# Performance work log

Measured on AMD Instinct MI355X. Metric: run time of the kernel, lower is better.

The kernel has to match this reference:

```python
import jax, jax.numpy as jnp
import numpy as np

N_NODES = 50000
N_EDGES = 200000
H = 128
L = 6
NODE_IN = 9
EDGE_IN = 10
OUT = 3


def _glorot(key, shape):
    fan_in = shape[0]
    return jax.random.normal(key, shape, dtype=jnp.float32) * (1.0 / np.sqrt(fan_in))


def setup_inputs() -> dict:
    key = jax.random.key(0)
    ks = jax.random.split(key, 32)
    x = jax.random.normal(ks[0], (N_NODES, NODE_IN), dtype=jnp.float32)
    edge_attr = jax.random.normal(ks[1], (N_EDGES, EDGE_IN), dtype=jnp.float32)
    edge_index = jax.random.randint(ks[2], (2, N_EDGES), 0, N_NODES, dtype=jnp.int32)
    bc_disp = (jax.random.uniform(ks[3], (N_NODES, 2)) < 0.05).astype(jnp.float32)
    bc_rot = (jax.random.uniform(ks[4], (N_NODES, 1)) < 0.05).astype(jnp.float32)
    inp = {
        'x': x, 'edge_attr': edge_attr, 'edge_index': edge_index,
        'bc_disp': bc_disp, 'bc_rot': bc_rot,
        # node encoder MLP(NODE_IN,[H],H)
        'enc_n_W1': _glorot(ks[5], (NODE_IN, H)), 'enc_n_b1': jnp.zeros((H,), jnp.float32),
        'enc_n_W2': _glorot(ks[6], (H, H)), 'enc_n_b2': jnp.zeros((H,), jnp.float32),
        # edge encoder MLP(EDGE_IN,[H],H)
        'enc_e_W1': _glorot(ks[7], (EDGE_IN, H)), 'enc_e_b1': jnp.zeros((H,), jnp.float32),
        'enc_e_W2': _glorot(ks[8], (H, H)), 'enc_e_b2': jnp.zeros((H,), jnp.float32),
        # L message-passing layers: msg MLP(3H->H->H), update MLP(2H->H->H), stacked on dim 0
        'mp_msg_W1': jnp.stack([_glorot(jax.random.fold_in(ks[9], i), (3 * H, H)) for i in range(L)]),
        'mp_msg_b1': jnp.zeros((L, H), jnp.float32),
        'mp_msg_W2': jnp.stack([_glorot(jax.random.fold_in(ks[10], i), (H, H)) for i in range(L)]),
        'mp_msg_b2': jnp.zeros((L, H), jnp.float32),
        'mp_upd_W1': jnp.stack([_glorot(jax.random.fold_in(ks[11], i), (2 * H, H)) for i in range(L)]),
        'mp_upd_b1': jnp.zeros((L, H), jnp.float32),
        'mp_upd_W2': jnp.stack([_glorot(jax.random.fold_in(ks[12], i), (H, H)) for i in range(L)]),
        'mp_upd_b2': jnp.zeros((L, H), jnp.float32),
        # decoder MLP(H,[H,64],OUT)
        'dec_W1': _glorot(ks[13], (H, H)), 'dec_b1': jnp.zeros((H,), jnp.float32),
        'dec_W2': _glorot(ks[14], (H, 64)), 'dec_b2': jnp.zeros((64,), jnp.float32),
        'dec_W3': _glorot(ks[15], (64, OUT)), 'dec_b3': jnp.zeros((OUT,), jnp.float32),
    }
    return inp


def _pignn_forward(x, edge_attr, edge_index, bc_disp, bc_rot,
                   enc_n_W1, enc_n_b1, enc_n_W2, enc_n_b2,
                   enc_e_W1, enc_e_b1, enc_e_W2, enc_e_b2,
                   mp_msg_W1, mp_msg_b1, mp_msg_W2, mp_msg_b2,
                   mp_upd_W1, mp_upd_b1, mp_upd_W2, mp_upd_b2,
                   dec_W1, dec_b1, dec_W2, dec_b2, dec_W3, dec_b3):
    relu = jax.nn.relu
    n = x.shape[0]
    src, dst = edge_index[0], edge_index[1]

    # encoders: Linear -> ReLU -> Linear
    h = relu(x @ enc_n_W1 + enc_n_b1) @ enc_n_W2 + enc_n_b2            # [N, H]
    e = relu(edge_attr @ enc_e_W1 + enc_e_b1) @ enc_e_W2 + enc_e_b2    # [E, H]

    def mp_step(h, params):
        mW1, mb1, mW2, mb2, uW1, ub1, uW2, ub2 = params
        m_in = jnp.concatenate([h[src], h[dst], e], axis=-1)           # [E, 3H]
        m = relu(m_in @ mW1 + mb1) @ mW2 + mb2                         # [E, H]
        agg = jax.ops.segment_sum(m, dst, num_segments=n)              # [N, H]
        u_in = jnp.concatenate([h, agg], axis=-1)                      # [N, 2H]
        upd = relu(u_in @ uW1 + ub1) @ uW2 + ub2                       # [N, H]
        return h + upd, None                                           # residual

    h, _ = jax.lax.scan(mp_step, h,
                        (mp_msg_W1, mp_msg_b1, mp_msg_W2, mp_msg_b2,
                         mp_upd_W1, mp_upd_b1, mp_upd_W2, mp_upd_b2))

    # decoder: H -> H -> 64 -> OUT with ReLU between layers
    d = relu(h @ dec_W1 + dec_b1)
    d = relu(d @ dec_W2 + dec_b2)
    pred = d @ dec_W3 + dec_b3                                         # [N, 3]

    # hard boundary conditions
    disp_mask = 1.0 - bc_disp
    rot_mask = 1.0 - bc_rot
    return jnp.concatenate([pred[:, 0:2] * disp_mask, pred[:, 2:3] * rot_mask], axis=1)


def reference(x, edge_attr, edge_index, bc_disp, bc_rot,
              enc_n_W1, enc_n_b1, enc_n_W2, enc_n_b2,
              enc_e_W1, enc_e_b1, enc_e_W2, enc_e_b2,
              mp_msg_W1, mp_msg_b1, mp_msg_W2, mp_msg_b2,
              mp_upd_W1, mp_upd_b1, mp_upd_W2, mp_upd_b2,
              dec_W1, dec_b1, dec_W2, dec_b2, dec_W3, dec_b3):
    return _pignn_forward(x, edge_attr, edge_index, bc_disp, bc_rot,
                          enc_n_W1, enc_n_b1, enc_n_W2, enc_n_b2,
                          enc_e_W1, enc_e_b1, enc_e_W2, enc_e_b2,
                          mp_msg_W1, mp_msg_b1, mp_msg_W2, mp_msg_b2,
                          mp_upd_W1, mp_upd_b1, mp_upd_W2, mp_upd_b2,
                          dec_W1, dec_b1, dec_W2, dec_b2, dec_W3, dec_b3)
```

## Files before the change

kernel.cpp:

```cpp
#include <hip/hip_runtime.h>

#define NN 50000
#define NE 200000
#define HD 128

typedef unsigned short us4 __attribute__((ext_vector_type(4)));
typedef unsigned short us8 __attribute__((ext_vector_type(8)));
typedef short s8 __attribute__((ext_vector_type(8)));
typedef float f4 __attribute__((ext_vector_type(4)));

#define SA 136
#define SA32 40
#define SC2 68

__device__ __forceinline__ float b2f(unsigned short u) {
    union { unsigned i; float f; } v; v.i = ((unsigned)u) << 16; return v.f;
}
__device__ __forceinline__ unsigned short f2b(float x) {
    union { float f; unsigned i; } v; v.f = x;
    unsigned r = v.i + 0x7fffu + ((v.i >> 16) & 1u);
    return (unsigned short)(r >> 16);
}
struct hl2 { short hi, lo; };
__device__ __forceinline__ hl2 split2(float x) {
    unsigned short h = f2b(x);
    hl2 r;
    r.hi = (short)h;
    r.lo = (short)f2b(x - b2f(h));
    return r;
}

__global__ __launch_bounds__(256) void zeroi_k(int* __restrict__ p, int n) {
    int i = blockIdx.x * 256 + threadIdx.x;
    if (i < n) p[i] = 0;
}
__global__ __launch_bounds__(256) void zerof_k(float* __restrict__ p, long n) {
    long i = (long)blockIdx.x * 256 + threadIdx.x;
    if (i < n) p[i] = 0.f;
}

__global__ __launch_bounds__(256) void hist_k(const int* __restrict__ dst, int* __restrict__ cnt) {
    int i = blockIdx.x * 256 + threadIdx.x;
    if (i < NE) atomicAdd(&cnt[dst[i]], 1);
}
__global__ __launch_bounds__(256) void scan1_k(const int* __restrict__ cnt, int* __restrict__ bsum) {
    __shared__ int sc[256];
    int i = blockIdx.x * 256 + threadIdx.x;
    sc[threadIdx.x] = (i < NN) ? cnt[i] : 0;
    __syncthreads();
    for (int off = 128; off > 0; off >>= 1) {
        if (threadIdx.x < off) sc[threadIdx.x] += sc[threadIdx.x + off];
        __syncthreads();
    }
    if (threadIdx.x == 0) bsum[blockIdx.x] = sc[0];
}
__global__ __launch_bounds__(256) void scan2_k(int* __restrict__ bsum, int nb) {
    __shared__ int sc[256];
    int t = threadIdx.x;
    int v = (t < nb) ? bsum[t] : 0;
    sc[t] = v;
    __syncthreads();
    for (int off = 1; off < 256; off <<= 1) {
        int a = (t >= off) ? sc[t - off] : 0;
        __syncthreads();
        sc[t] += a;
        __syncthreads();
    }
    if (t < nb) bsum[t] = sc[t] - v;
}
__global__ __launch_bounds__(256) void scan3_k(const int* __restrict__ cnt, const int* __restrict__ bsum,
                                               int* __restrict__ rp, float* __restrict__ deg) {
    __shared__ int sc[256];
    int t = threadIdx.x;
    int i = blockIdx.x * 256 + t;
    int v = (i < NN) ? cnt[i] : 0;
    sc[t] = v;
    __syncthreads();
    for (int off = 1; off < 256; off <<= 1) {
        int a = (t >= off) ? sc[t - off] : 0;
        __syncthreads();
        sc[t] += a;
        __syncthreads();
    }
    int incl = sc[t];
    if (i < NN) {
        rp[i] = bsum[blockIdx.x] + incl - v;
        deg[i] = (float)v;
        if (i == NN - 1) rp[NN] = bsum[blockIdx.x] + incl;
    }
}
__global__ __launch_bounds__(256) void posbuild_k(const int* __restrict__ src, const int* __restrict__ dst,
                                                  const int* __restrict__ rp, int* __restrict__ cur,
                                                  int* __restrict__ pos, int* __restrict__ srcS,
                                                  int* __restrict__ dstS) {
    int i = blockIdx.x * 256 + threadIdx.x;
    if (i >= NE) return;
    int d = dst[i];
    int p = rp[d] + atomicAdd(&cur[d], 1);
    pos[i] = p;
    srcS[p] = src[i];
    dstS[p] = d;
}

__global__ __launch_bounds__(256) void mini_k(const float* __restrict__ W2m, const float* __restrict__ uW1b,
                                              const float* __restrict__ b2m,
                                              float* __restrict__ W2u, float* __restrict__ b2u) {
    int r = blockIdx.x * 16 + (threadIdx.x >> 4);
    int c0 = (threadIdx.x & 15) * 8;
    float a[8] = {};
    for (int k = 0; k < HD; ++k) {
        float w = W2m[r * HD + k];
        const float* u = uW1b + k * HD + c0;
        float4 u0 = *(const float4*)u, u1 = *(const float4*)(u + 4);
        a[0] = fmaf(w, u0.x, a[0]); a[1] = fmaf(w, u0.y, a[1]);
        a[2] = fmaf(w, u0.z, a[2]); a[3] = fmaf(w, u0.w, a[3]);
        a[4] = fmaf(w, u1.x, a[4]); a[5] = fmaf(w, u1.y, a[5]);
        a[6] = fmaf(w, u1.z, a[6]); a[7] = fmaf(w, u1.w, a[7]);
    }
    *(float4*)(W2u + r * HD + c0)     = float4{a[0], a[1], a[2], a[3]};
    *(float4*)(W2u + r * HD + c0 + 4) = float4{a[4], a[5], a[6], a[7]};
    if (blockIdx.x == 0 && threadIdx.x < 16) {
        int cc = threadIdx.x * 8;
        float b[8] = {};
        for (int k = 0; k < HD; ++k) {
            float w = b2m[k];
            const float* u = uW1b + k * HD + cc;
            float4 u0 = *(const float4*)u, u1 = *(const float4*)(u + 4);
            b[0] = fmaf(w, u0.x, b[0]); b[1] = fmaf(w, u0.y, b[1]);
            b[2] = fmaf(w, u0.z, b[2]); b[3] = fmaf(w, u0.w, b[3]);
            b[4] = fmaf(w, u1.x, b[4]); b[5] = fmaf(w, u1.y, b[5]);
            b[6] = fmaf(w, u1.z, b[6]); b[7] = fmaf(w, u1.w, b[7]);
        }
        *(float4*)(b2u + cc)     = float4{b[0], b[1], b[2], b[3]};
        *(float4*)(b2u + cc + 4) = float4{b[4], b[5], b[6], b[7]};
    }
}
__global__ __launch_bounds__(256) void wtL_k(const float* __restrict__ msgW1, const float* __restrict__ updW1,
                                             const float* __restrict__ updW2, const float* __restrict__ W2uF,
                                             unsigned short* __restrict__ dst) {
    int idx = blockIdx.x * 256 + threadIdx.x;
    int m = idx >> 14;
    int r = idx & 16383;
    int n = r >> 7, k = r & 127;
    float v;
    switch (m) {
        case 0: v = msgW1[(long)k * HD + n]; break;
        case 1: v = msgW1[(long)(128 + k) * HD + n]; break;
        case 2: v = msgW1[(long)(256 + k) * HD + n]; break;
        case 3: v = updW1[(long)k * HD + n]; break;
        case 4: v = updW2[(long)k * HD + n]; break;
        default: v = W2uF[(long)k * HD + n]; break;
    }
    hl2 p = split2(v);
    dst[(long)m * 32768 + n * HD + k] = (unsigned short)p.hi;
    dst[(long)m * 32768 + 16384 + n * HD + k] = (unsigned short)p.lo;
}
__global__ __launch_bounds__(256) void wtE_k(const float* __restrict__ nW1, const float* __restrict__ nW2,
                                             const float* __restrict__ eW1, const float* __restrict__ eW2,
                                             unsigned short* __restrict__ dst) {
    int idx = blockIdx.x * 256 + threadIdx.x;
    float v; long off; int pos, sz;
    if (idx < 4096) {
        int n = idx >> 5, k = idx & 31;
        v = (k < 9) ? nW1[k * HD + n] : 0.f; off = 0; pos = idx; sz = 4096;
    } else if (idx < 20480) {
        int r = idx - 4096; int n = r >> 7, k = r & 127;
        v = nW2[k * HD + n]; off = 8192; pos = r; sz = 16384;
    } else if (idx < 24576) {
        int r = idx - 20480; int n = r >> 5, k = r & 31;
        v = (k < 10) ? eW1[k * HD + n] : 0.f; off = 40960; pos = r; sz = 4096;
    } else {
        int r = idx - 24576; int n = r >> 7, k = r & 127;
        v = eW2[k * HD + n]; off = 49152; pos = r; sz = 16384;
    }
    hl2 p = split2(v);
    dst[off + pos] = (unsigned short)p.hi;
    dst[off + sz + pos] = (unsigned short)p.lo;
}
__global__ __launch_bounds__(256) void wtD_k(const float* __restrict__ dW1, const float* __restrict__ dW2,
                                             unsigned short* __restrict__ dst) {
    int idx = blockIdx.x * 256 + threadIdx.x;
    if (idx < 16384) {
        int n = idx >> 7, k = idx & 127;
        hl2 p = split2(dW1[k * HD + n]);
        dst[idx] = (unsigned short)p.hi;
        dst[16384 + idx] = (unsigned short)p.lo;
    } else {
        int r = idx - 16384;
        int n = r >> 7, k = r & 127;
        hl2 p = split2(dW2[k * 64 + n]);
        dst[32768 + r] = (unsigned short)p.hi;
        dst[40960 + r] = (unsigned short)p.lo;
    }
}

__device__ __forceinline__ void stageA_f32_split(short* __restrict__ At, short* __restrict__ Al,
                                                 const float* __restrict__ A, int bm, int M, int tid) {
#pragma unroll
    for (int t = 0; t < 4; ++t) {
        int c = tid + t * 256;
        int row = c >> 4, k8 = (c & 15) * 8;
        int gr = bm + row;
        s8 vh = (s8)0, vl = (s8)0;
        if (gr < M) {
            const float* p = A + (long)gr * HD + k8;
            f4 a = *(const f4*)p, b = *(const f4*)(p + 4);
#pragma unroll
            for (int i = 0; i < 4; ++i) {
                hl2 pa = split2(a[i]);
                hl2 pb = split2(b[i]);
                vh[i] = pa.hi; vl[i] = pa.lo;
                vh[4 + i] = pb.hi; vl[4 + i] = pb.lo;
            }
        }
        *(s8*)(At + row * SA + k8) = vh;
        *(s8*)(Al + row * SA + k8) = vl;
    }
}
__device__ __forceinline__ void stageA_b16(short* __restrict__ At, const unsigned short* __restrict__ A,
                                           int bm, int M, int tid) {
#pragma unroll
    for (int t = 0; t < 4; ++t) {
        int c = tid + t * 256;
        int row = c >> 4, k8 = (c & 15) * 8;
        int gr = bm + row;
        s8 v = (s8)0;
        if (gr < M) v = *(const s8*)(A + (long)gr * HD + k8);
        *(s8*)(At + row * SA + k8) = v;
    }
}
__device__ __forceinline__ void loadB2(s8 b[2][4], const unsigned short* __restrict__ W,
                                       int sw, int nk, int w, int lane) {
    const int r16 = lane & 15, q8 = (lane >> 4) * 8;
#pragma unroll
    for (int ct = 0; ct < 2; ++ct)
#pragma unroll 4
        for (int ks = 0; ks < nk; ++ks)
            b[ct][ks] = *(const s8*)((const short*)W + (long)((2 * w + ct) * 16 + r16) * sw + ks * 32 + q8);
}
__device__ __forceinline__ void mfma3_reg(f4 acc[4][2], const short* __restrict__ At,
                                          const short* __restrict__ Al, int sa,
                                          const s8 bh[2][4], const s8 bl[2][4], int nk, int lane) {
    const int r16 = lane & 15, q8 = (lane >> 4) * 8;
#pragma unroll 4
    for (int ks = 0; ks < nk; ++ks)
#pragma unroll
        for (int rt = 0; rt < 4; ++rt) {
            s8 ah = *(const s8*)(At + (rt * 16 + r16) * sa + ks * 32 + q8);
            s8 al = *(const s8*)(Al + (rt * 16 + r16) * sa + ks * 32 + q8);
#pragma unroll
            for (int ct = 0; ct < 2; ++ct) {
                acc[rt][ct] = __builtin_amdgcn_mfma_f32_16x16x32_bf16(ah, bh[ct][ks], acc[rt][ct], 0, 0, 0);
                acc[rt][ct] = __builtin_amdgcn_mfma_f32_16x16x32_bf16(al, bh[ct][ks], acc[rt][ct], 0, 0, 0);
                acc[rt][ct] = __builtin_amdgcn_mfma_f32_16x16x32_bf16(ah, bl[ct][ks], acc[rt][ct], 0, 0, 0);
            }
        }
}
__device__ __forceinline__ void mfmaE_reg(f4 acc[4][2], const short* __restrict__ At, int sa,
                                          const s8 bh[2][4], const s8 bl[2][4], int nk, int lane) {
    const int r16 = lane & 15, q8 = (lane >> 4) * 8;
#pragma unroll 4
    for (int ks = 0; ks < nk; ++ks)
#pragma unroll
        for (int rt = 0; rt < 4; ++rt) {
            s8 a = *(const s8*)(At + (rt * 16 + r16) * sa + ks * 32 + q8);
#pragma unroll
            for (int ct = 0; ct < 2; ++ct) {
                acc[rt][ct] = __builtin_amdgcn_mfma_f32_16x16x32_bf16(a, bh[ct][ks], acc[rt][ct], 0, 0, 0);
                acc[rt][ct] = __builtin_amdgcn_mfma_f32_16x16x32_bf16(a, bl[ct][ks], acc[rt][ct], 0, 0, 0);
            }
        }
}
__device__ __forceinline__ void dumpC_half2(float* __restrict__ Cd, const f4 acc[4][2],
                                            int half, int w, int lane) {
    if ((w >> 1) != half) return;
    const int col0 = lane & 15, rq = (lane >> 4) * 4;
    const int bc = (w & 1) * 2;
#pragma unroll
    for (int rt = 0; rt < 4; ++rt)
#pragma unroll
        for (int ct = 0; ct < 2; ++ct)
#pragma unroll
            for (int r = 0; r < 4; ++r)
                Cd[(rt * 16 + rq + r) * SC2 + (bc + ct) * 16 + col0] = acc[rt][ct][r];
}
#define ACC_ZERO2(acc) { f4 z_ = {0.f, 0.f, 0.f, 0.f}; \
    for (int r_ = 0; r_ < 4; ++r_) for (int c_ = 0; c_ < 2; ++c_) acc[r_][c_] = z_; }

__device__ __forceinline__ void stageA32_f32(short* __restrict__ At, short* __restrict__ Al,
                                             const float* __restrict__ A, int bm, int M, int tid) {
#pragma unroll
    for (int t = 0; t < 2; ++t) {
        int c = tid + t * 256;
        int row = c >> 4, k8 = (c & 15) * 8;
        int gr = bm + row;
        s8 vh = (s8)0, vl = (s8)0;
        if (gr < M) {
            const float* p = A + (long)gr * HD + k8;
            f4 a = *(const f4*)p, b = *(const f4*)(p + 4);
#pragma unroll
            for (int i = 0; i < 4; ++i) {
                hl2 pa = split2(a[i]);
                hl2 pb = split2(b[i]);
                vh[i] = pa.hi; vl[i] = pa.lo;
                vh[4 + i] = pb.hi; vl[4 + i] = pb.lo;
            }
        }
        *(s8*)(At + row * SA + k8) = vh;
        *(s8*)(Al + row * SA + k8) = vl;
    }
}
__device__ __forceinline__ void stage_segsum32(short* __restrict__ At, short* __restrict__ Al,
                                               const unsigned short* __restrict__ Pe,
                                               const int* __restrict__ rowp,
                                               int bm, int M, int tid) {
#pragma unroll
    for (int t = 0; t < 2; ++t) {
        int c = tid + t * 256;
        int row = c >> 4, k8 = (c & 15) * 8;
        int gr = bm + row;
        float sum[8] = {};
        if (gr < M) {
            int e0 = rowp[gr], e1 = rowp[gr + 1];
            int e = e0;
            for (; e + 2 <= e1; e += 2) {
                us8 v0 = *(const us8*)(Pe + (long)e * HD + k8);
                us8 v1 = *(const us8*)(Pe + (long)(e + 1) * HD + k8);
#pragma unroll
                for (int i = 0; i < 8; ++i) sum[i] += b2f(v0[i]) + b2f(v1[i]);
            }
            if (e < e1) {
                us8 v = *(const us8*)(Pe + (long)e * HD + k8);
#pragma unroll
                for (int i = 0; i < 8; ++i) sum[i] += b2f(v[i]);
            }
        }
        s8 vh, vl;
#pragma unroll
        for (int i = 0; i < 8; ++i) {
            hl2 p = split2(sum[i]);
            vh[i] = p.hi; vl[i] = p.lo;
        }
        *(s8*)(At + row * SA + k8) = vh;
        *(s8*)(Al + row * SA + k8) = vl;
    }
}
__device__ __forceinline__ void mfma3_reg32(f4 acc[2][2], const short* __restrict__ At,
                                            const short* __restrict__ Al,
                                            const s8 bh[2][4], const s8 bl[2][4], int lane) {
    const int r16 = lane & 15, q8 = (lane >> 4) * 8;
#pragma unroll
    for (int ks = 0; ks < 4; ++ks)
#pragma unroll
        for (int rt = 0; rt < 2; ++rt) {
            s8 ah = *(const s8*)(At + (rt * 16 + r16) * SA + ks * 32 + q8);
            s8 al = *(const s8*)(Al + (rt * 16 + r16) * SA + ks * 32 + q8);
#pragma unroll
            for (int ct = 0; ct < 2; ++ct) {
                acc[rt][ct] = __builtin_amdgcn_mfma_f32_16x16x32_bf16(ah, bh[ct][ks], acc[rt][ct], 0, 0, 0);
                acc[rt][ct] = __builtin_amdgcn_mfma_f32_16x16x32_bf16(al, bh[ct][ks], acc[rt][ct], 0, 0, 0);
                acc[rt][ct] = __builtin_amdgcn_mfma_f32_16x16x32_bf16(ah, bl[ct][ks], acc[rt][ct], 0, 0, 0);
            }
        }
}
__device__ __forceinline__ void dumpC32(float* __restrict__ Cd, const f4 acc[2][2],
                                        int half, int w, int lane) {
    if ((w >> 1) != half) return;
    const int col0 = lane & 15, rq = (lane >> 4) * 4;
    const int bc = (w & 1) * 2;
#pragma unroll
    for (int rt = 0; rt < 2; ++rt)
#pragma unroll
        for (int ct = 0; ct < 2; ++ct)
#pragma unroll
            for (int r = 0; r < 4; ++r)
                Cd[(rt * 16 + rq + r) * SC2 + (bc + ct) * 16 + col0] = acc[rt][ct][r];
}
#define ACC_ZERO22(acc) { f4 z_ = {0.f, 0.f, 0.f, 0.f}; \
    for (int r_ = 0; r_ < 2; ++r_) for (int c_ = 0; c_ < 2; ++c_) acc[r_][c_] = z_; }

__global__ __launch_bounds__(256) void dual_k(const float* __restrict__ h,
                                              const unsigned short* __restrict__ W1aT,
                                              const unsigned short* __restrict__ W1bT,
                                              unsigned short* __restrict__ Hs, unsigned short* __restrict__ Hd,
                                              int M) {
    __shared__ __align__(16) short At[64 * SA];
    __shared__ __align__(16) short Al[64 * SA];
    __shared__ __align__(16) float Cd[64 * SC2];
    const int tid = threadIdx.x, lane = tid & 63, w = tid >> 6, tx = tid & 15, ty = tid >> 4;
    const int bm = blockIdx.x * 64;
    s8 bh[2][4], bl[2][4];
    loadB2(bh, W1aT, HD, 4, w, lane);
    loadB2(bl, W1aT + 16384, HD, 4, w, lane);
    stageA_f32_split(At, Al, h, bm, M, tid);
    __syncthreads();
    f4 acc[4][2]; ACC_ZERO2(acc);
    mfma3_reg(acc, At, Al, SA, bh, bl, 4, lane);
    loadB2(bh, W1bT, HD, 4, w, lane);
    loadB2(bl, W1bT + 16384, HD, 4, w, lane);
#pragma unroll
    for (int half = 0; half < 2; ++half) {
        __syncthreads();
        dumpC_half2(Cd, acc, half, w, lane);
        __syncthreads();
        int c4 = half * 64 + tx * 4;
#pragma unroll
        for (int i = 0; i < 4; ++i) {
            int row = ty * 4 + i, gr = bm + row;
            if (gr >= M) continue;
            f4 v = *(const f4*)(Cd + row * SC2 + tx * 4);
            us4 o;
#pragma unroll
            for (int j = 0; j < 4; ++j) o[j] = f2b(v[j]);
            *(us4*)(Hs + (long)gr * HD + c4) = o;
        }
    }
    ACC_ZERO2(acc);
    mfma3_reg(acc, At, Al, SA, bh, bl, 4, lane);
#pragma unroll
    for (int half = 0; half < 2; ++half) {
        __syncthreads();
        dumpC_half2(Cd, acc, half, w, lane);
        __syncthreads();
        int c4 = half * 64 + tx * 4;
#pragma unroll
        for (int i = 0; i < 4; ++i) {
            int row = ty * 4 + i, gr = bm + row;
            if (gr >= M) continue;
            f4 v = *(const f4*)(Cd + row * SC2 + tx * 4);
            us4 o;
#pragma unroll
            for (int j = 0; j < 4; ++j) o[j] = f2b(v[j]);
            *(us4*)(Hd + (long)gr * HD + c4) = o;
        }
    }
}

__global__ __launch_bounds__(256) void edge_k(const unsigned short* __restrict__ eS,
                                              const unsigned short* __restrict__ Hs,
                                              const unsigned short* __restrict__ Hd,
                                              const int* __restrict__ srcS, const int* __restrict__ dstS,
                                              const unsigned short* __restrict__ W1cT,
                                              const float* __restrict__ b1,
                                              unsigned short* __restrict__ Pe) {
    __shared__ __align__(16) short At[64 * SA];
    __shared__ __align__(16) float Cd[64 * SC2];
    const int tid = threadIdx.x, lane = tid & 63, w = tid >> 6, tx = tid & 15, ty = tid >> 4;
    const int bm = blockIdx.x * 64;
    s8 bh[2][4], bl[2][4];
    loadB2(bh, W1cT, HD, 4, w, lane);
    loadB2(bl, W1cT + 16384, HD, 4, w, lane);
    stageA_b16(At, eS, bm, NE, tid);
    __syncthreads();
    f4 acc[4][2]; ACC_ZERO2(acc);
    mfmaE_reg(acc, At, SA, bh, bl, 4, lane);
#pragma unroll
    for (int half = 0; half < 2; ++half) {
        __syncthreads();
        dumpC_half2(Cd, acc, half, w, lane);
        __syncthreads();
        int c4 = half * 64 + tx * 4;
        f4 bv = *(const f4*)(b1 + c4);
#pragma unroll
        for (int i = 0; i < 4; ++i) {
            int row = ty * 4 + i, edge = bm + row;
            int s = srcS[edge], d = dstS[edge];
            us4 hs = *(const us4*)(Hs + (long)s * HD + c4);
            us4 hd = *(const us4*)(Hd + (long)d * HD + c4);
            f4 cv = *(const f4*)(Cd + row * SC2 + tx * 4);
            us4 o;
#pragma unroll
            for (int j = 0; j < 4; ++j)
                o[j] = f2b(fmaxf(cv[j] + bv[j] + b2f(hs[j]) + b2f(hd[j]), 0.f));
            *(us4*)(Pe + (long)edge * HD + c4) = o;
        }
    }
}

__global__ __launch_bounds__(256) void upd_k(float* __restrict__ h,
                                             const unsigned short* __restrict__ Pe,
                                             const int* __restrict__ rowp,
                                             const unsigned short* __restrict__ uW1aT,
                                             const unsigned short* __restrict__ W2uT,
                                             const float* __restrict__ ub1, const float* __restrict__ b2u,
                                             const float* __restrict__ deg,
                                             const unsigned short* __restrict__ uW2T,
                                             const float* __restrict__ ub2,
                                             const unsigned short* __restrict__ W1aTn,
                                             const unsigned short* __restrict__ W1bTn,
                                             unsigned short* __restrict__ Hs,
                                             unsigned short* __restrict__ Hd, int M) {
    __shared__ __align__(16) short At[32 * SA];
    __shared__ __align__(16) short Al[32 * SA];
    __shared__ __align__(16) float Cd[32 * SC2];
    const int tid = threadIdx.x, lane = tid & 63, w = tid >> 6, tx = tid & 15, ty = tid >> 4;
    const int bm = blockIdx.x * 32;
    const int col0 = lane & 15, rq = (lane >> 4) * 4;
    s8 bh[2][4], bl[2][4];
    f4 acc[2][2]; ACC_ZERO22(acc);
    loadB2(bh, uW1aT, HD, 4, w, lane);
    loadB2(bl, uW1aT + 16384, HD, 4, w, lane);
    stageA32_f32(At, Al, h, bm, M, tid);
    __syncthreads();
    mfma3_reg32(acc, At, Al, bh, bl, lane);
    loadB2(bh, W2uT, HD, 4, w, lane);
    loadB2(bl, W2uT + 16384, HD, 4, w, lane);
    __syncthreads();
    stage_segsum32(At, Al, Pe, rowp, bm, M, tid);
    __syncthreads();
    mfma3_reg32(acc, At, Al, bh, bl, lane);
    loadB2(bh, uW2T, HD, 4, w, lane);
    loadB2(bl, uW2T + 16384, HD, 4, w, lane);
    __syncthreads();
    {
        float u1[2], u2[2];
#pragma unroll
        for (int ct = 0; ct < 2; ++ct) {
            int col = (2 * w + ct) * 16 + col0;
            u1[ct] = ub1[col]; u2[ct] = b2u[col];
        }
        float dgv[8];
#pragma unroll
        for (int rt = 0; rt < 2; ++rt)
#pragma unroll
            for (int r = 0; r < 4; ++r) {
                int gr = bm + rt * 16 + rq + r;
                dgv[rt * 4 + r] = (gr < M) ? deg[gr] : 0.f;
            }
#pragma unroll
        for (int rt = 0; rt < 2; ++rt)
#pragma unroll
            for (int ct = 0; ct < 2; ++ct)
#pragma unroll
                for (int r = 0; r < 4; ++r) {
                    float p = fmaxf(acc[rt][ct][r] + u1[ct] + dgv[rt * 4 + r] * u2[ct], 0.f);
                    hl2 pp = split2(p);
                    int off = (rt * 16 + rq + r) * SA + (2 * w + ct) * 16 + col0;
                    At[off] = pp.hi;
                    Al[off] = pp.lo;
                }
    }
    __syncthreads();
    ACC_ZERO22(acc);
    mfma3_reg32(acc, At, Al, bh, bl, lane);
    if (W1aTn) {
        loadB2(bh, W1aTn, HD, 4, w, lane);
        loadB2(bl, W1aTn + 16384, HD, 4, w, lane);
    }
    __syncthreads();
#pragma unroll
    for (int half = 0; half < 2; ++half) {
        __syncthreads();
        dumpC32(Cd, acc, half, w, lane);
        __syncthreads();
        int c4 = half * 64 + tx * 4;
        f4 u0 = *(const f4*)(ub2 + c4);
#pragma unroll
        for (int i = 0; i < 2; ++i) {
            int row = ty * 2 + i, gr = bm + row;
            if (gr >= M) continue;
            float* hp = h + (long)gr * HD + c4;
            f4 a = *(f4*)hp;
            f4 cv = *(const f4*)(Cd + row * SC2 + tx * 4);
#pragma unroll
            for (int j = 0; j < 4; ++j) a[j] += cv[j] + u0[j];
            *(f4*)hp = a;
#pragma unroll
            for (int j = 0; j < 4; ++j) {
                hl2 pp = split2(a[j]);
                At[row * SA + c4 + j] = pp.hi;
                Al[row * SA + c4 + j] = pp.lo;
            }
        }
    }
    if (!W1aTn) return;
    __syncthreads();
    ACC_ZERO22(acc);
    mfma3_reg32(acc, At, Al, bh, bl, lane);
    loadB2(bh, W1bTn, HD, 4, w, lane);
    loadB2(bl, W1bTn + 16384, HD, 4, w, lane);
#pragma unroll
    for (int half = 0; half < 2; ++half) {
        __syncthreads();
        dumpC32(Cd, acc, half, w, lane);
        __syncthreads();
        int c4 = half * 64 + tx * 4;
#pragma unroll
        for (int i = 0; i < 2; ++i) {
            int row = ty * 2 + i, gr = bm + row;
            if (gr >= M) continue;
            f4 v = *(const f4*)(Cd + row * SC2 + tx * 4);
            us4 o;
#pragma unroll
            for (int j = 0; j < 4; ++j) o[j] = f2b(v[j]);
            *(us4*)(Hs + (long)gr * HD + c4) = o;
        }
    }
    ACC_ZERO22(acc);
    mfma3_reg32(acc, At, Al, bh, bl, lane);
#pragma unroll
    for (int half = 0; half < 2; ++half) {
        __syncthreads();
        dumpC32(Cd, acc, half, w, lane);
        __syncthreads();
        int c4 = half * 64 + tx * 4;
#pragma unroll
        for (int i = 0; i < 2; ++i) {
            int row = ty * 2 + i, gr = bm + row;
            if (gr >= M) continue;
            f4 v = *(const f4*)(Cd + row * SC2 + tx * 4);
            us4 o;
#pragma unroll
            for (int j = 0; j < 4; ++j) o[j] = f2b(v[j]);
            *(us4*)(Hd + (long)gr * HD + c4) = o;
        }
    }
}

template<bool SCAT>
__global__ __launch_bounds__(256) void enc_k(const float* __restrict__ A, int KIN,
                                             const unsigned short* __restrict__ W1T, const float* __restrict__ b1,
                                             const unsigned short* __restrict__ W2T, const float* __restrict__ b2,
                                             float* __restrict__ outF, unsigned short* __restrict__ outB,
                                             const int* __restrict__ pos, int M) {
    __shared__ __align__(16) short At[64 * SA];
    __shared__ __align__(16) short Al[64 * SA];
    float* Cd = (float*)At;
    const int tid = threadIdx.x, lane = tid & 63, w = tid >> 6, tx = tid & 15, ty = tid >> 4;
    const int bm = blockIdx.x * 64;
    s8 bh[2][4], bl[2][4];
    loadB2(bh, W1T, 32, 1, w, lane);
    loadB2(bl, W1T + 4096, 32, 1, w, lane);
    {
        int row = tid >> 2, k8 = (tid & 3) * 8;
        int gr = bm + row;
        s8 vh = (s8)0, vl = (s8)0;
        if (gr < M) {
#pragma unroll
            for (int i = 0; i < 8; ++i) {
                int k = k8 + i;
                if (k < KIN) {
                    hl2 p = split2(A[(long)gr * KIN + k]);
                    vh[i] = p.hi; vl[i] = p.lo;
                }
            }
        }
        *(s8*)(At + row * SA32 + k8) = vh;
        *(s8*)(Al + row * SA32 + k8) = vl;
    }
    __syncthreads();
    f4 acc[4][2]; ACC_ZERO2(acc);
    mfma3_reg(acc, At, Al, SA32, bh, bl, 1, lane);
    loadB2(bh, W2T, HD, 4, w, lane);
    loadB2(bl, W2T + 16384, HD, 4, w, lane);
    __syncthreads();
    {
        const int col0 = lane & 15, rq = (lane >> 4) * 4;
        float bb[2];
#pragma unroll
        for (int ct = 0; ct < 2; ++ct) bb[ct] = b1[(2 * w + ct) * 16 + col0];
#pragma unroll
        for (int rt = 0; rt < 4; ++rt)
#pragma unroll
            for (int ct = 0; ct < 2; ++ct)
#pragma unroll
                for (int r = 0; r < 4; ++r) {
                    float p = fmaxf(acc[rt][ct][r] + bb[ct], 0.f);
                    hl2 pp = split2(p);
                    int off = (rt * 16 + rq + r) * SA + (2 * w + ct) * 16 + col0;
                    At[off] = pp.hi;
                    Al[off] = pp.lo;
                }
    }
    __syncthreads();
    ACC_ZERO2(acc);
    mfma3_reg(acc, At, Al, SA, bh, bl, 4, lane);
#pragma unroll
    for (int half = 0; half < 2; ++half) {
        __syncthreads();
        dumpC_half2(Cd, acc, half, w, lane);
        __syncthreads();
        int c4 = half * 64 + tx * 4;
        f4 bv = *(const f4*)(b2 + c4);
#pragma unroll
        for (int i = 0; i < 4; ++i) {
            int row = ty * 4 + i, gr = bm + row;
            if (gr >= M) continue;
            f4 cv = *(const f4*)(Cd + row * SC2 + tx * 4);
            if constexpr (SCAT) {
                int p = pos[gr];
                us4 o;
#pragma unroll
                for (int j = 0; j < 4; ++j) o[j] = f2b(cv[j] + bv[j]);
                *(us4*)(outB + (long)p * HD + c4) = o;
            } else {
                f4 o;
#pragma unroll
                for (int j = 0; j < 4; ++j) o[j] = cv[j] + bv[j];
                *(f4*)(outF + (long)gr * HD + c4) = o;
            }
        }
    }
}

__global__ __launch_bounds__(256) void dec2_k(const float* __restrict__ h,
                                              const unsigned short* __restrict__ WtD,
                                              const float* __restrict__ b1, const float* __restrict__ b2,
                                              const float* __restrict__ W3, const float* __restrict__ b3,
                                              const float* __restrict__ bc_disp, const float* __restrict__ bc_rot,
                                              float* __restrict__ outp, int M) {
    __shared__ __align__(16) short At[64 * SA];
    __shared__ __align__(16) short Al[64 * SA];
    float* D2 = (float*)At;
    const int tid = threadIdx.x, lane = tid & 63, w = tid >> 6;
    const int bm = blockIdx.x * 64;
    s8 bh[2][4], bl[2][4];
    loadB2(bh, WtD, HD, 4, w, lane);
    loadB2(bl, WtD + 16384, HD, 4, w, lane);
    stageA_f32_split(At, Al, h, bm, M, tid);
    __syncthreads();
    f4 acc[4][2]; ACC_ZERO2(acc);
    mfma3_reg(acc, At, Al, SA, bh, bl, 4, lane);
    __syncthreads();
    {
        const int col0 = lane & 15, rq = (lane >> 4) * 4;
        float bb[2];
#pragma unroll
        for (int ct = 0; ct < 2; ++ct) bb[ct] = b1[(2 * w + ct) * 16 + col0];
#pragma unroll
        for (int rt = 0; rt < 4; ++rt)
#pragma unroll
            for (int ct = 0; ct < 2; ++ct)
#pragma unroll
                for (int r = 0; r < 4; ++r) {
                    float p = fmaxf(acc[rt][ct][r] + bb[ct], 0.f);
                    hl2 pp = split2(p);
                    int off = (rt * 16 + rq + r) * SA + (2 * w + ct) * 16 + col0;
                    At[off] = pp.hi;
                    Al[off] = pp.lo;
                }
    }
    __syncthreads();
    const int r16 = lane & 15, q8 = (lane >> 4) * 8, rq = (lane >> 4) * 4;
    f4 acc2[4];
    { f4 z_ = {0.f, 0.f, 0.f, 0.f}; for (int r_ = 0; r_ < 4; ++r_) acc2[r_] = z_; }
    {
        s8 b2h[4], b2l[4];
#pragma unroll
        for (int ks = 0; ks < 4; ++ks) {
            b2h[ks] = *(const s8*)((const short*)WtD + 32768 + (long)(w * 16 + r16) * HD + ks * 32 + q8);
            b2l[ks] = *(const s8*)((const short*)WtD + 40960 + (long)(w * 16 + r16) * HD + ks * 32 + q8);
        }
#pragma unroll
        for (int ks = 0; ks < 4; ++ks)
#pragma unroll
            for (int rt = 0; rt < 4; ++rt) {
                s8 ah = *(const s8*)(At + (rt * 16 + r16) * SA + ks * 32 + q8);
                s8 al = *(const s8*)(Al + (rt * 16 + r16) * SA + ks * 32 + q8);
                acc2[rt] = __builtin_amdgcn_mfma_f32_16x16x32_bf16(ah, b2h[ks], acc2[rt], 0, 0, 0);
                acc2[rt] = __builtin_amdgcn_mfma_f32_16x16x32_bf16(al, b2h[ks], acc2[rt], 0, 0, 0);
                acc2[rt] = __builtin_amdgcn_mfma_f32_16x16x32_bf16(ah, b2l[ks], acc2[rt], 0, 0, 0);
            }
    }
    __syncthreads();
    {
        float b2v = b2[w * 16 + r16];
#pragma unroll
        for (int rt = 0; rt < 4; ++rt)
#pragma unroll
            for (int r = 0; r < 4; ++r)
                D2[(rt * 16 + rq + r) * 65 + w * 16 + r16] = fmaxf(acc2[rt][r] + b2v, 0.f);
    }
    __syncthreads();
    if (tid < 64) {
        int gr = bm + tid;
        if (gr < M) {
            float a0 = b3[0], a1 = b3[1], a2 = b3[2];
#pragma unroll
            for (int k = 0; k < 64; ++k) {
                float v = D2[tid * 65 + k];
                a0 = fmaf(v, W3[k * 3 + 0], a0);
                a1 = fmaf(v, W3[k * 3 + 1], a1);
                a2 = fmaf(v, W3[k * 3 + 2], a2);
            }
            outp[gr * 3 + 0] = a0 * (1.f - bc_disp[gr * 2 + 0]);
            outp[gr * 3 + 1] = a1 * (1.f - bc_disp[gr * 2 + 1]);
            outp[gr * 3 + 2] = a2 * (1.f - bc_rot[gr]);
        }
    }
}

extern "C" void kernel_launch(void* const* d_in, const int* in_sizes, int n_in,
                              void* d_out, int out_size, void* d_ws, size_t ws_size,
                              hipStream_t stream)
{
    const float* x        = (const float*)d_in[0];
    const float* eattr    = (const float*)d_in[1];
    const int*   eidx     = (const int*)d_in[2];
    const float* bc_disp  = (const float*)d_in[3];
    const float* bc_rot   = (const float*)d_in[4];
    const float* enc_n_W1 = (const float*)d_in[5];
    const float* enc_n_b1 = (const float*)d_in[6];
    const float* enc_n_W2 = (const float*)d_in[7];
    const float* enc_n_b2 = (const float*)d_in[8];
    const float* enc_e_W1 = (const float*)d_in[9];
    const float* enc_e_b1 = (const float*)d_in[10];
    const float* enc_e_W2 = (const float*)d_in[11];
    const float* enc_e_b2 = (const float*)d_in[12];
    const float* msg_W1   = (const float*)d_in[13];
    const float* msg_b1   = (const float*)d_in[14];
    const float* msg_W2   = (const float*)d_in[15];
    const float* msg_b2   = (const float*)d_in[16];
    const float* upd_W1   = (const float*)d_in[17];
    const float* upd_b1   = (const float*)d_in[18];
    const float* upd_W2   = (const float*)d_in[19];
    const float* upd_b2   = (const float*)d_in[20];
    const float* dec_W1   = (const float*)d_in[21];
    const float* dec_b1   = (const float*)d_in[22];
    const float* dec_W2   = (const float*)d_in[23];
    const float* dec_b2   = (const float*)d_in[24];
    const float* dec_W3   = (const float*)d_in[25];
    const float* dec_b3   = (const float*)d_in[26];

    const int* src = eidx;
    const int* dst = eidx + NE;

    char* base = (char*)d_ws;
    float* h  = (float*)base;
    unsigned short* Hs = (unsigned short*)(h + (long)NN * HD);
    unsigned short* Hd = Hs + (long)NN * HD;
    unsigned short* eS = Hd + (long)NN * HD;
    unsigned short* Pe = eS + (long)NE * HD;
    float* W2uF = (float*)(Pe + (long)NE * HD);
    float* b2uA = W2uF + 6 * HD * HD;
    unsigned short* WtL = (unsigned short*)(b2uA + 6 * HD);
    unsigned short* WtE = WtL + 6L * 6 * 32768;
    unsigned short* WtD = WtE + 81920;
    float* deg = (float*)(WtD + 49152);
    int* rowp  = (int*)(deg + NN);
    int* cnt   = rowp + (NN + 1);
    int* posb  = cnt + NN;
    int* srcS  = posb + NE;
    int* dstS  = srcS + NE;
    int* bsum  = dstS + NE;
    size_t need = (size_t)((char*)(bsum + 256) - base);
    if (ws_size < need) {
        zerof_k<<<(unsigned)((out_size + 255) / 256), 256, 0, stream>>>((float*)d_out, out_size);
        return;
    }

    dim3 blk(256);
    const unsigned gN   = (NN + 63) / 64;
    const unsigned gN32 = (NN + 31) / 32;
    const unsigned gE   = NE / 64;
    const unsigned gNc  = (NN + 255) / 256;
    const unsigned gEc  = (NE + 255) / 256;

    zeroi_k<<<gNc, blk, 0, stream>>>(cnt, NN);
    hist_k<<<gEc, blk, 0, stream>>>(dst, cnt);
    scan1_k<<<gNc, blk, 0, stream>>>(cnt, bsum);
    scan2_k<<<1, blk, 0, stream>>>(bsum, (int)gNc);
    scan3_k<<<gNc, blk, 0, stream>>>(cnt, bsum, rowp, deg);
    zeroi_k<<<gNc, blk, 0, stream>>>(cnt, NN);
    posbuild_k<<<gEc, blk, 0, stream>>>(src, dst, rowp, cnt, posb, srcS, dstS);

    for (int l = 0; l < 6; ++l) {
        mini_k<<<8, blk, 0, stream>>>(msg_W2 + (long)l * HD * HD,
                                      upd_W1 + (long)l * 256 * HD + 128 * HD,
                                      msg_b2 + (long)l * HD,
                                      W2uF + (long)l * HD * HD, b2uA + (long)l * HD);
    }
    for (int l = 0; l < 6; ++l) {
        wtL_k<<<384, blk, 0, stream>>>(msg_W1 + (long)l * 384 * HD,
                                       upd_W1 + (long)l * 256 * HD,
                                       upd_W2 + (long)l * HD * HD,
                                       W2uF + (long)l * HD * HD,
                                       WtL + (long)l * 6 * 32768);
    }
    wtE_k<<<160, blk, 0, stream>>>(enc_n_W1, enc_n_W2, enc_e_W1, enc_e_W2, WtE);
    wtD_k<<<96, blk, 0, stream>>>(dec_W1, dec_W2, WtD);

    enc_k<false><<<gN, blk, 0, stream>>>(x, 9, WtE, enc_n_b1, WtE + 8192, enc_n_b2,
                                         h, nullptr, nullptr, NN);
    enc_k<true><<<gE, blk, 0, stream>>>(eattr, 10, WtE + 40960, enc_e_b1, WtE + 49152, enc_e_b2,
                                        nullptr, eS, posb, NE);

    dual_k<<<gN, blk, 0, stream>>>(h, WtL + 0L * 32768, WtL + 1L * 32768, Hs, Hd, NN);
    for (int l = 0; l < 6; ++l) {
        const unsigned short* Wt = WtL + (long)l * 6 * 32768;
        const float* b1  = msg_b1 + (long)l * HD;
        const float* ub1 = upd_b1 + (long)l * HD;
        const float* ub2 = upd_b2 + (long)l * HD;
        const float* b2u = b2uA + (long)l * HD;
        const unsigned short* Wn = (l < 5) ? (WtL + (long)(l + 1) * 6 * 32768) : nullptr;

        edge_k<<<gE, blk, 0, stream>>>(eS, Hs, Hd, srcS, dstS, Wt + 2L * 32768, b1, Pe);
        upd_k<<<gN32, blk, 0, stream>>>(h, Pe, rowp, Wt + 3L * 32768, Wt + 5L * 32768,
                                        ub1, b2u, deg, Wt + 4L * 32768, ub2,
                                        Wn, Wn ? (Wn + 32768) : nullptr, Hs, Hd, NN);
    }

    dec2_k<<<gN, blk, 0, stream>>>(h, WtD, dec_b1, dec_b2, dec_W3, dec_b3,
                                   bc_disp, bc_rot, (float*)d_out, NN);
}
```

Measured before the change: 1.049 ms.

## Double-buffer upd_k staging and dump full C tile to cut barriers

Adds a second pair of split-bf16 LDS buffers so the h tile and the segment-summed messages are staged together before one barrier, and the two MFMA passes run back to back without a sync between them. The epilogues now dump the whole 32x128 accumulator into a wider LDS buffer in one pass instead of two halves, which drops several __syncthreads and lets the stores use wider 8-element bf16 writes. The cost is more LDS per block, which may reduce occupancy, and the aggregation's global loads are issued earlier, which raises register pressure.

```diff
diff --git a/kernel.cpp b/kernel.cpp
--- a/kernel.cpp
+++ b/kernel.cpp
@@ -12,6 +12,7 @@
 #define SA 136
 #define SA32 40
 #define SC2 68
+#define SC 132
 
 __device__ __forceinline__ float b2f(unsigned short u) {
     union { unsigned i; float f; } v; v.i = ((unsigned)u) << 16; return v.f;
@@ -310,7 +311,7 @@
         *(s8*)(Al + row * SA + k8) = vl;
     }
 }
-__device__ __forceinline__ void stage_segsum32(short* __restrict__ At, short* __restrict__ Al,
+__device__ __forceinline__ void stage_segsum32(short* __restrict__ Bt, short* __restrict__ Bl,
                                                const unsigned short* __restrict__ Pe,
                                                const int* __restrict__ rowp,
                                                int bm, int M, int tid) {
@@ -341,8 +342,8 @@
             hl2 p = split2(sum[i]);
             vh[i] = p.hi; vl[i] = p.lo;
         }
-        *(s8*)(At + row * SA + k8) = vh;
-        *(s8*)(Al + row * SA + k8) = vl;
+        *(s8*)(Bt + row * SA + k8) = vh;
+        *(s8*)(Bl + row * SA + k8) = vl;
     }
 }
 __device__ __forceinline__ void mfma3_reg32(f4 acc[2][2], const short* __restrict__ At,
@@ -363,18 +364,16 @@
             }
         }
 }
-__device__ __forceinline__ void dumpC32(float* __restrict__ Cd, const f4 acc[2][2],
-                                        int half, int w, int lane) {
-    if ((w >> 1) != half) return;
+__device__ __forceinline__ void dumpC32_full(float* __restrict__ Cd, const f4 acc[2][2],
+                                             int w, int lane) {
     const int col0 = lane & 15, rq = (lane >> 4) * 4;
-    const int bc = (w & 1) * 2;
 #pragma unroll
     for (int rt = 0; rt < 2; ++rt)
 #pragma unroll
         for (int ct = 0; ct < 2; ++ct)
 #pragma unroll
             for (int r = 0; r < 4; ++r)
-                Cd[(rt * 16 + rq + r) * SC2 + (bc + ct) * 16 + col0] = acc[rt][ct][r];
+                Cd[(rt * 16 + rq + r) * SC + (2 * w + ct) * 16 + col0] = acc[rt][ct][r];
 }
 #define ACC_ZERO22(acc) { f4 z_ = {0.f, 0.f, 0.f, 0.f}; \
     for (int r_ = 0; r_ < 2; ++r_) for (int c_ = 0; c_ < 2; ++c_) acc[r_][c_] = z_; }
@@ -492,8 +491,10 @@
                                              unsigned short* __restrict__ Hd, int M) {
     __shared__ __align__(16) short At[32 * SA];
     __shared__ __align__(16) short Al[32 * SA];
-    __shared__ __align__(16) float Cd[32 * SC2];
-    const int tid = threadIdx.x, lane = tid & 63, w = tid >> 6, tx = tid & 15, ty = tid >> 4;
+    __shared__ __align__(16) short Bt[32 * SA];
+    __shared__ __align__(16) short Bl[32 * SA];
+    __shared__ __align__(16) float Cd[32 * SC];
+    const int tid = threadIdx.x, lane = tid & 63, w = tid >> 6;
     const int bm = blockIdx.x * 32;
     const int col0 = lane & 15, rq = (lane >> 4) * 4;
     s8 bh[2][4], bl[2][4];
@@ -501,14 +502,12 @@
     loadB2(bh, uW1aT, HD, 4, w, lane);
     loadB2(bl, uW1aT + 16384, HD, 4, w, lane);
     stageA32_f32(At, Al, h, bm, M, tid);
+    stage_segsum32(Bt, Bl, Pe, rowp, bm, M, tid);
     __syncthreads();
     mfma3_reg32(acc, At, Al, bh, bl, lane);
     loadB2(bh, W2uT, HD, 4, w, lane);
     loadB2(bl, W2uT + 16384, HD, 4, w, lane);
-    __syncthreads();
-    stage_segsum32(At, Al, Pe, rowp, bm, M, tid);
-    __syncthreads();
-    mfma3_reg32(acc, At, Al, bh, bl, lane);
+    mfma3_reg32(acc, Bt, Bl, bh, bl, lane);
     loadB2(bh, uW2T, HD, 4, w, lane);
     loadB2(bl, uW2T + 16384, HD, 4, w, lane);
     __syncthreads();
@@ -547,73 +546,73 @@
         loadB2(bh, W1aTn, HD, 4, w, lane);
         loadB2(bl, W1aTn + 16384, HD, 4, w, lane);
     }
-    __syncthreads();
-#pragma unroll
-    for (int half = 0; half < 2; ++half) {
-        __syncthreads();
-        dumpC32(Cd, acc, half, w, lane);
-        __syncthreads();
-        int c4 = half * 64 + tx * 4;
-        f4 u0 = *(const f4*)(ub2 + c4);
-#pragma unroll
-        for (int i = 0; i < 2; ++i) {
-            int row = ty * 2 + i, gr = bm + row;
-            if (gr >= M) continue;
-            float* hp = h + (long)gr * HD + c4;
-            f4 a = *(f4*)hp;
-            f4 cv = *(const f4*)(Cd + row * SC2 + tx * 4);
-#pragma unroll
-            for (int j = 0; j < 4; ++j) a[j] += cv[j] + u0[j];
-            *(f4*)hp = a;
+    dumpC32_full(Cd, acc, w, lane);
+    __syncthreads();
+#pragma unroll
+    for (int t = 0; t < 4; ++t) {
+        int idx = tid + t * 256;
+        int row = idx >> 5, q = idx & 31;
+        int gr = bm + row;
+        if (gr >= M) {
 #pragma unroll
             for (int j = 0; j < 4; ++j) {
-                hl2 pp = split2(a[j]);
-                At[row * SA + c4 + j] = pp.hi;
-                Al[row * SA + c4 + j] = pp.lo;
-            }
+                Bt[row * SA + q * 4 + j] = 0;
+                Bl[row * SA + q * 4 + j] = 0;
+            }
+            continue;
+        }
+        f4 cv = *(const f4*)(Cd + row * SC + q * 4);
+        f4 u0 = *(const f4*)(ub2 + q * 4);
+        float* hp = h + (long)gr * HD + q * 4;
+        f4 a = *(f4*)hp;
+#pragma unroll
+        for (int j = 0; j < 4; ++j) a[j] += cv[j] + u0[j];
+        *(f4*)hp = a;
+#pragma unroll
+        for (int j = 0; j < 4; ++j) {
+            hl2 pp = split2(a[j]);
+            Bt[row * SA + q * 4 + j] = pp.hi;
+            Bl[row * SA + q * 4 + j] = pp.lo;
         }
     }
     if (!W1aTn) return;
     __syncthreads();
     ACC_ZERO22(acc);
-    mfma3_reg32(acc, At, Al, bh, bl, lane);
+    mfma3_reg32(acc, Bt, Bl, bh, bl, lane);
     loadB2(bh, W1bTn, HD, 4, w, lane);
     loadB2(bl, W1bTn + 16384, HD, 4, w, lane);
-#pragma unroll
-    for (int half = 0; half < 2; ++half) {
-        __syncthreads();
-        dumpC32(Cd, acc, half, w, lane);
-        __syncthreads();
-        int c4 = half * 64 + tx * 4;
-#pragma unroll
-        for (int i = 0; i < 2; ++i) {
-            int row = ty * 2 + i, gr = bm + row;
-            if (gr >= M) continue;
-            f4 v = *(const f4*)(Cd + row * SC2 + tx * 4);
-            us4 o;
-#pragma unroll
-            for (int j = 0; j < 4; ++j) o[j] = f2b(v[j]);
-            *(us4*)(Hs + (long)gr * HD + c4) = o;
-        }
-    }
+    dumpC32_full(Cd, acc, w, lane);
+    __syncthreads();
+#pragma unroll
+    for (int t = 0; t < 2; ++t) {
+        int idx = tid + t * 256;
+        int row = idx >> 4, k8 = (idx & 15) * 8;
+        int gr = bm + row;
+        if (gr >= M) continue;
+        f4 c0 = *(const f4*)(Cd + row * SC + k8);
+        f4 c1 = *(const f4*)(Cd + row * SC + k8 + 4);
+        us8 o;
+#pragma unroll
+        for (int j = 0; j < 4; ++j) { o[j] = f2b(c0[j]); o[4 + j] = f2b(c1[j]); }
+        *(us8*)(Hs + (long)gr * HD + k8) = o;
+    }
+    __syncthreads();
     ACC_ZERO22(acc);
-    mfma3_reg32(acc, At, Al, bh, bl, lane);
-#pragma unroll
-    for (int half = 0; half < 2; ++half) {
-        __syncthreads();
-        dumpC32(Cd, acc, half, w, lane);
-        __syncthreads();
-        int c4 = half * 64 + tx * 4;
-#pragma unroll
-        for (int i = 0; i < 2; ++i) {
-            int row = ty * 2 + i, gr = bm + row;
-            if (gr >= M) continue;
-            f4 v = *(const f4*)(Cd + row * SC2 + tx * 4);
-            us4 o;
-#pragma unroll
-            for (int j = 0; j < 4; ++j) o[j] = f2b(v[j]);
-            *(us4*)(Hd + (long)gr * HD + c4) = o;
-        }
+    mfma3_reg32(acc, Bt, Bl, bh, bl, lane);
+    dumpC32_full(Cd, acc, w, lane);
+    __syncthreads();
+#pragma unroll
+    for (int t = 0; t < 2; ++t) {
+        int idx = tid + t * 256;
+        int row = idx >> 4, k8 = (idx & 15) * 8;
+        int gr = bm + row;
+        if (gr >= M) continue;
+        f4 c0 = *(const f4*)(Cd + row * SC + k8);
+        f4 c1 = *(const f4*)(Cd + row * SC + k8 + 4);
+        us8 o;
+#pragma unroll
+        for (int j = 0; j < 4; ++j) { o[j] = f2b(c0[j]); o[4 + j] = f2b(c1[j]); }
+        *(us8*)(Hd + (long)gr * HD + k8) = o;
     }
 }
 
```

Result: no change. 1.036 ms (-1.3%).
